# Kernel tuning notes

Hardware: AMD Instinct MI355X
Metric: run time of the kernel (lower is better)

## Reference

```python
import jax, jax.numpy as jnp
import numpy as np

N = 50000          # padded nodes
E_CFG = 800000     # padded cfg edges
E_GKT = 800000     # padded gkt edges
FN = 128           # node feature dim
FE = 128           # gkt edge feature dim
OUT = 128          # out_size (== hidden dim, required by shared Linears)
HEADS = 8
HEAD = OUT // HEADS
DIN = FN + OUT     # input dim to shared Linears


def _seg_softmax(logits, seg_ids, num_segments):
    mx = jax.ops.segment_max(logits, seg_ids, num_segments=num_segments)
    e = jnp.exp(logits - mx[seg_ids])
    s = jax.ops.segment_sum(e, seg_ids, num_segments=num_segments)
    return e / s[seg_ids]


def setup_inputs() -> dict:
    key = jax.random.key(0)
    ks = jax.random.split(key, 16)
    d = {
        'node_fts': jax.random.normal(ks[0], (N, FN), jnp.float32),
        'gkt_edge_fts': jax.random.normal(ks[1], (E_GKT, FE), jnp.float32),
        'hidden': jax.random.normal(ks[2], (N, OUT), jnp.float32),
        'cfg_indices_padded': jax.random.randint(ks[3], (E_CFG, 2), 0, N, jnp.int32),
        'gkt_indices_padded': jax.random.randint(ks[4], (E_GKT, 2), 0, N, jnp.int32),
    }
    sc = 1.0 / np.sqrt(DIN)
    d['W_m'] = jax.random.normal(ks[5], (DIN, OUT), jnp.float32) * sc
    d['b_m'] = jnp.zeros((OUT,), jnp.float32)
    d['W_skip'] = jax.random.normal(ks[6], (DIN, OUT), jnp.float32) * sc
    d['b_skip'] = jnp.zeros((OUT,), jnp.float32)
    d['W_a1'] = jax.random.normal(ks[7], (DIN, HEADS), jnp.float32) * sc
    d['b_a1'] = jnp.zeros((HEADS,), jnp.float32)
    d['W_a2'] = jax.random.normal(ks[8], (DIN, HEADS), jnp.float32) * sc
    d['b_a2'] = jnp.zeros((HEADS,), jnp.float32)
    d['W_ae'] = jax.random.normal(ks[9], (FE, HEADS), jnp.float32) * (1.0 / np.sqrt(FE))
    d['b_ae'] = jnp.zeros((HEADS,), jnp.float32)
    return d


def reference(node_fts, gkt_edge_fts, hidden, cfg_indices_padded, gkt_indices_padded,
              W_m, b_m, W_skip, b_skip, W_a1, b_a1, W_a2, b_a2, W_ae, b_ae):
    nb_nodes = node_fts.shape[0]
    nb_cfg = cfg_indices_padded.shape[0]
    nb_gkt = gkt_indices_padded.shape[0]
    cfg_row, cfg_col = cfg_indices_padded[:, 0], cfg_indices_padded[:, 1]
    gkt_row, gkt_col = gkt_indices_padded[:, 0], gkt_indices_padded[:, 1]

    # ---- cfg pass ----
    cfg_z = jnp.concatenate([node_fts, hidden], axis=-1)           # [N, DIN]
    cfg_att1 = cfg_z @ W_a1 + b_a1                                 # [N, H]
    cfg_att2 = cfg_z @ W_a2 + b_a2
    cfg_logits = cfg_att1[cfg_row] + cfg_att2[cfg_col]             # [E, H]
    cfg_coefs = _seg_softmax(jax.nn.leaky_relu(cfg_logits), cfg_row, nb_cfg)
    cfg_vals = (cfg_z @ W_m + b_m).reshape(nb_nodes, HEADS, HEAD)  # [N, H, hd]
    cfg_msg = cfg_coefs[:, :, None] * cfg_vals[cfg_col]            # [E, H, hd]
    cfg_hidden = jax.ops.segment_sum(cfg_msg, cfg_row, num_segments=nb_nodes)
    cfg_hidden = cfg_hidden.reshape(nb_nodes, OUT)
    cfg_hidden = cfg_hidden + (cfg_z @ W_skip + b_skip)            # residual
    cfg_hidden = jax.nn.relu(cfg_hidden)

    # ---- gkt pass ----
    gkt_z = jnp.concatenate([node_fts, cfg_hidden], axis=-1)       # [N, DIN]
    gkt_att1 = gkt_z @ W_a1 + b_a1
    gkt_att2 = gkt_z @ W_a2 + b_a2
    gkt_att_e = gkt_edge_fts @ W_ae + b_ae                         # [E, H]
    gkt_logits = gkt_att1[gkt_row] + gkt_att2[gkt_col] + gkt_att_e
    gkt_coefs = _seg_softmax(jax.nn.leaky_relu(gkt_logits), gkt_row, nb_gkt)
    gkt_vals = (gkt_z @ W_m + b_m).reshape(nb_nodes, HEADS, HEAD)
    msg = gkt_coefs[:, :, None] * gkt_vals[gkt_col]
    ret = jax.ops.segment_sum(msg, gkt_row, num_segments=nb_nodes)
    ret = ret.reshape(nb_nodes, OUT)
    ret = ret + (gkt_z @ W_skip + b_skip)
    ret = jax.nn.relu(ret)
    return ret
```

## Files before the change

kernel.cpp:

```cpp
#include <hip/hip_runtime.h>

using short8  = __attribute__((ext_vector_type(8))) short;
using floatx4 = __attribute__((ext_vector_type(4))) float;

#define CAP 64

__device__ __forceinline__ unsigned short f2bf(float f) {
    unsigned int u = __float_as_uint(f);
    u += 0x7fffu + ((u >> 16) & 1u);
    return (unsigned short)(u >> 16);
}
__device__ __forceinline__ float bf2f(unsigned short s) {
    return __uint_as_float(((unsigned int)s) << 16);
}

__global__ void k_prep(const float* __restrict__ Wm, const float* __restrict__ Wsk,
                       const float* __restrict__ Wa1, const float* __restrict__ Wa2,
                       unsigned short* __restrict__ Wpack, float* __restrict__ Wa,
                       const float* __restrict__ nf, const float* __restrict__ hid,
                       unsigned short* __restrict__ zbf,
                       int* __restrict__ cur0, int* __restrict__ cur1, int N) {
    int id = blockIdx.x * 256 + threadIdx.x;
    if (id < 65536) {
        int col = id >> 8;
        int k = id & 255;
        float v = (col < 128) ? Wm[k * 128 + col] : Wsk[k * 128 + (col - 128)];
        Wpack[col * 256 + k] = f2bf(v);
        if (id < 256 * 16) {
            int kk = id >> 4, j = id & 15;
            Wa[kk * 16 + j] = (j < 8) ? Wa1[kk * 8 + j] : Wa2[kk * 8 + (j - 8)];
        }
    }
    if (id < N) { cur0[id] = id * CAP; cur1[id] = id * CAP; }
    if (id >= N * 32) return;
    int row = id >> 5;
    int c4 = (id & 31) * 4;
    float4 av = *(const float4*)&nf[row * 128 + c4];
    float4 bv = *(const float4*)&hid[row * 128 + c4];
    ushort4 pa; pa.x = f2bf(av.x); pa.y = f2bf(av.y); pa.z = f2bf(av.z); pa.w = f2bf(av.w);
    ushort4 pb; pb.x = f2bf(bv.x); pb.y = f2bf(bv.y); pb.z = f2bf(bv.z); pb.w = f2bf(bv.w);
    *(ushort4*)&zbf[row * 256 + c4] = pa;
    *(ushort4*)&zbf[row * 256 + 128 + c4] = pb;
}

__global__ void k_fill_both(const int* __restrict__ cfg_idx, const int* __restrict__ gkt_idx,
                            int* __restrict__ cur0, int* __restrict__ cur1,
                            int* __restrict__ ccol, int2* __restrict__ ce, int Ec, int Eg) {
    int e = blockIdx.x * 256 + threadIdx.x;
    if (e < Ec) {
        int r = cfg_idx[2 * e], c = cfg_idx[2 * e + 1];
        int p = atomicAdd(&cur0[r], 1);
        if (p < r * CAP + CAP) ccol[p] = c;
    }
    if (e < Eg) {
        int r = gkt_idx[2 * e], c = gkt_idx[2 * e + 1];
        int p = atomicAdd(&cur1[r], 1);
        if (p < r * CAP + CAP) { int2 v; v.x = c; v.y = e; ce[p] = v; }
    }
}

__launch_bounds__(256)
__global__ void k_gemm(const unsigned short* __restrict__ zbf,
                       const unsigned short* __restrict__ Wpack,
                       const float* __restrict__ bm, const float* __restrict__ bsk,
                       unsigned short* __restrict__ vals, float* __restrict__ skip, int M) {
    const int colblk = blockIdx.x;
    const int rowBase = blockIdx.y * 128;
    __shared__ short As[128 * 40];
    __shared__ short Bs[128 * 40];
    const int t = threadIdx.x;
    const int wid = t >> 6, lane = t & 63;
    const int wm = wid >> 1, wn = wid & 1;

    floatx4 acc[4][4];
#pragma unroll
    for (int i = 0; i < 4; i++)
#pragma unroll
        for (int j = 0; j < 4; j++) acc[i][j] = (floatx4){0.f, 0.f, 0.f, 0.f};

    const unsigned short* Bbase = Wpack + colblk * 128 * 256;
    const int kq = (lane >> 4) * 8;
    const int rr = lane & 15;

    for (int kt = 0; kt < 256; kt += 32) {
#pragma unroll
        for (int s = 0; s < 2; s++) {
            int ch = t + s * 256;
            int r = ch >> 2, c = ch & 3;
            int gr = rowBase + r; if (gr >= M) gr = M - 1;
            *(int4*)&As[r * 40 + c * 8] = *(const int4*)&zbf[gr * 256 + kt + c * 8];
            *(int4*)&Bs[r * 40 + c * 8] = *(const int4*)&Bbase[r * 256 + kt + c * 8];
        }
        __syncthreads();
        short8 af[4], bfm[4];
#pragma unroll
        for (int i = 0; i < 4; i++) af[i] = *(short8*)&As[(wm * 64 + i * 16 + rr) * 40 + kq];
#pragma unroll
        for (int j = 0; j < 4; j++) bfm[j] = *(short8*)&Bs[(wn * 64 + j * 16 + rr) * 40 + kq];
#pragma unroll
        for (int i = 0; i < 4; i++)
#pragma unroll
            for (int j = 0; j < 4; j++)
                acc[i][j] = __builtin_amdgcn_mfma_f32_16x16x32_bf16(af[i], bfm[j], acc[i][j], 0, 0, 0);
        __syncthreads();
    }

    const int rquad = lane >> 4, cidx = lane & 15;
#pragma unroll
    for (int i = 0; i < 4; i++) {
#pragma unroll
        for (int j = 0; j < 4; j++) {
            int gc = wn * 64 + j * 16 + cidx;
#pragma unroll
            for (int r = 0; r < 4; r++) {
                int gr = rowBase + wm * 64 + i * 16 + rquad * 4 + r;
                if (gr < M) {
                    float v = acc[i][j][r];
                    if (colblk == 0) vals[gr * 128 + gc] = f2bf(v + bm[gc]);
                    else             skip[gr * 128 + gc] = v + bsk[gc];
                }
            }
        }
    }
}

__launch_bounds__(256)
__global__ void k_att(const float* __restrict__ zA, const float* __restrict__ zB,
                      const float* __restrict__ Wa, const float* __restrict__ ba1,
                      const float* __restrict__ ba2, float* __restrict__ att, int N) {
    __shared__ float Ws[4096];
    int t = threadIdx.x;
#pragma unroll
    for (int s = 0; s < 16; s++) Ws[s * 256 + t] = Wa[s * 256 + t];
    __syncthreads();
    int node = blockIdx.x * 256 + t;
    if (node >= N) return;
    float acc[16];
#pragma unroll
    for (int j = 0; j < 16; j++) acc[j] = (j < 8) ? ba1[j] : ba2[j - 8];
    const float* a = &zA[node * 128];
    const float* b = &zB[node * 128];
    for (int k0 = 0; k0 < 128; k0 += 4) {
        float4 v = *(const float4*)&a[k0];
        float vv[4] = {v.x, v.y, v.z, v.w};
#pragma unroll
        for (int r = 0; r < 4; r++) {
            const float* w = &Ws[(k0 + r) * 16];
#pragma unroll
            for (int j = 0; j < 16; j++) acc[j] += vv[r] * w[j];
        }
    }
    for (int k0 = 0; k0 < 128; k0 += 4) {
        float4 v = *(const float4*)&b[k0];
        float vv[4] = {v.x, v.y, v.z, v.w};
#pragma unroll
        for (int r = 0; r < 4; r++) {
            const float* w = &Ws[(128 + k0 + r) * 16];
#pragma unroll
            for (int j = 0; j < 16; j++) acc[j] += vv[r] * w[j];
        }
    }
#pragma unroll
    for (int j = 0; j < 16; j++) att[node * 16 + j] = acc[j];
}

__launch_bounds__(256)
__global__ void k_atte(const float* __restrict__ ef, const float* __restrict__ Wae,
                       const float* __restrict__ bae, float* __restrict__ atte, int E) {
    __shared__ float Ws[1024];
    int t = threadIdx.x;
    for (int s = t; s < 1024; s += 256) Ws[s] = Wae[s];
    __syncthreads();
    int e = blockIdx.x * 256 + t;
    if (e >= E) return;
    float acc[8];
#pragma unroll
    for (int h = 0; h < 8; h++) acc[h] = bae[h];
    const float* row = &ef[e * 128];
    for (int k0 = 0; k0 < 128; k0 += 4) {
        float4 v = *(const float4*)&row[k0];
        float vv[4] = {v.x, v.y, v.z, v.w};
#pragma unroll
        for (int r = 0; r < 4; r++) {
            const float* w = &Ws[(k0 + r) * 8];
#pragma unroll
            for (int h = 0; h < 8; h++) acc[h] += vv[r] * w[h];
        }
    }
    float4 o0 = {acc[0], acc[1], acc[2], acc[3]};
    float4 o1 = {acc[4], acc[5], acc[6], acc[7]};
    *(float4*)&atte[e * 8] = o0;
    *(float4*)&atte[e * 8 + 4] = o1;
}

template <int PHASE>
__launch_bounds__(256)
__global__ void k_agg(const int* __restrict__ cursor,
                      const int* __restrict__ ccol, const int2* __restrict__ ce,
                      const float* __restrict__ att, const unsigned short* __restrict__ vals,
                      const float* __restrict__ skip, const float* __restrict__ atte,
                      unsigned short* __restrict__ zbf, float* __restrict__ cfgh,
                      float* __restrict__ out, int N) {
    int node = (blockIdx.x * 256 + threadIdx.x) >> 6;
    int lane = threadIdx.x & 63;
    if (node >= N) return;
    int h = lane >> 3;
    int f0 = lane * 2;
    int base = node * CAP;
    int cnt = cursor[node] - base;
    if (cnt > CAP) cnt = CAP;
    if (cnt < 0) cnt = 0;

    int mycol = 0, myeid = 0;
    if (lane < cnt) {
        if (PHASE == 0) mycol = ccol[base + lane];
        else { int2 v = ce[base + lane]; mycol = v.x; myeid = v.y; }
    }
    float a1 = att[node * 16 + h];
    float acc0 = 0.f, acc1 = 0.f, dsum = 0.f;
#pragma unroll 4
    for (int s = 0; s < cnt; s++) {
        int col = __shfl(mycol, s);
        float logit = a1 + att[col * 16 + 8 + h];
        if (PHASE == 1) {
            int eid = __shfl(myeid, s);
            logit += atte[eid * 8 + h];
        }
        float l = (logit >= 0.f) ? logit : 0.01f * logit;
        float w = __expf(l);
        dsum += w;
        unsigned int pv = *(const unsigned int*)&vals[col * 128 + f0];
        acc0 += w * bf2f((unsigned short)(pv & 0xffffu));
        acc1 += w * bf2f((unsigned short)(pv >> 16));
    }
    if (cnt > 0) {
        float inv = 1.f / dsum;
        acc0 *= inv; acc1 *= inv;
    }
    float r0 = acc0 + skip[node * 128 + f0];
    float r1 = acc1 + skip[node * 128 + f0 + 1];
    r0 = r0 > 0.f ? r0 : 0.f;
    r1 = r1 > 0.f ? r1 : 0.f;
    if (PHASE == 0) {
        unsigned int packed = ((unsigned int)f2bf(r1) << 16) | (unsigned int)f2bf(r0);
        *(unsigned int*)&zbf[node * 256 + 128 + f0] = packed;
        float2 fo = {r0, r1};
        *(float2*)&cfgh[node * 128 + f0] = fo;
    } else {
        float2 fo = {r0, r1};
        *(float2*)&out[node * 128 + f0] = fo;
    }
}

extern "C" void kernel_launch(void* const* d_in, const int* in_sizes, int n_in,
                              void* d_out, int out_size, void* d_ws, size_t ws_size,
                              hipStream_t stream) {
    const float* node_fts = (const float*)d_in[0];
    const float* gkt_ef   = (const float*)d_in[1];
    const float* hidden   = (const float*)d_in[2];
    const int*   cfg_idx  = (const int*)d_in[3];
    const int*   gkt_idx  = (const int*)d_in[4];
    const float* W_m  = (const float*)d_in[5];
    const float* b_m  = (const float*)d_in[6];
    const float* W_sk = (const float*)d_in[7];
    const float* b_sk = (const float*)d_in[8];
    const float* W_a1 = (const float*)d_in[9];
    const float* b_a1 = (const float*)d_in[10];
    const float* W_a2 = (const float*)d_in[11];
    const float* b_a2 = (const float*)d_in[12];
    const float* W_ae = (const float*)d_in[13];
    const float* b_ae = (const float*)d_in[14];

    const int N  = in_sizes[0] / 128;
    const int Ec = in_sizes[3] / 2;
    const int Eg = in_sizes[4] / 2;
    const int Emax = (Ec > Eg) ? Ec : Eg;

    char* ws = (char*)d_ws;
    size_t off = 0;
    auto alloc = [&](size_t bytes) -> void* {
        off = (off + 255) & ~(size_t)255;
        void* p = ws + off;
        off += bytes;
        return p;
    };
    unsigned short* zbf   = (unsigned short*)alloc((size_t)N * 256 * 2);
    unsigned short* vals  = (unsigned short*)alloc((size_t)N * 128 * 2);
    float* skip   = (float*)alloc((size_t)N * 128 * 4);
    float* cfgh   = (float*)alloc((size_t)N * 128 * 4);
    float* att    = (float*)alloc((size_t)N * 16 * 4);
    float* atte   = (float*)alloc((size_t)Eg * 8 * 4);
    unsigned short* Wpack = (unsigned short*)alloc(256 * 256 * 2);
    float* Wa     = (float*)alloc(256 * 16 * 4);
    int* cur0     = (int*)alloc((size_t)N * 4);
    int* cur1     = (int*)alloc((size_t)N * 4);
    int* ccol     = (int*)alloc((size_t)N * CAP * 4);
    int2* ce      = (int2*)alloc((size_t)N * CAP * 8);

    dim3 ggrid(2, (N + 127) / 128);

    k_prep<<<(N * 32 + 255) / 256, 256, 0, stream>>>(W_m, W_sk, W_a1, W_a2, Wpack, Wa,
                                                     node_fts, hidden, zbf, cur0, cur1, N);
    k_fill_both<<<(Emax + 255) / 256, 256, 0, stream>>>(cfg_idx, gkt_idx, cur0, cur1,
                                                        ccol, ce, Ec, Eg);
    k_atte<<<(Eg + 255) / 256, 256, 0, stream>>>(gkt_ef, W_ae, b_ae, atte, Eg);

    k_gemm<<<ggrid, 256, 0, stream>>>(zbf, Wpack, b_m, b_sk, vals, skip, N);
    k_att<<<(N + 255) / 256, 256, 0, stream>>>(node_fts, hidden, Wa, b_a1, b_a2, att, N);
    k_agg<0><<<(N * 64 + 255) / 256, 256, 0, stream>>>(cur0, ccol, nullptr, att, vals,
                                                       skip, nullptr, zbf, cfgh, nullptr, N);

    k_gemm<<<ggrid, 256, 0, stream>>>(zbf, Wpack, b_m, b_sk, vals, skip, N);
    k_att<<<(N + 255) / 256, 256, 0, stream>>>(node_fts, cfgh, Wa, b_a1, b_a2, att, N);
    k_agg<1><<<(N * 64 + 255) / 256, 256, 0, stream>>>(cur1, nullptr, ce, att, vals,
                                                       skip, atte, nullptr, nullptr,
                                                       (float*)d_out, N);
}
```

Measured before the change: 1.023 ms.

## Precompute per-edge softmax weights in CSR slots before aggregation

Moves the attention-logit and exp computation out of the aggregation loop into per-edge kernels that write weights directly into the CSR slot layout. The cfg weights are computed during the fill (after computing att earlier), and the gkt edge-feature projection is fused with logit and exp into one kernel that also skips edges beyond capacity. Aggregation then streams contiguous weights instead of gathering att rows and edge logits. This adds two large weight buffers (N*CAP*8 floats each) and a pos1 array, which means extra memory traffic and footprint.

```diff
diff --git a/kernel.cpp b/kernel.cpp
--- a/kernel.cpp
+++ b/kernel.cpp
@@ -43,20 +43,89 @@
     *(ushort4*)&zbf[row * 256 + 128 + c4] = pb;
 }
 
-__global__ void k_fill_both(const int* __restrict__ cfg_idx, const int* __restrict__ gkt_idx,
-                            int* __restrict__ cur0, int* __restrict__ cur1,
-                            int* __restrict__ ccol, int2* __restrict__ ce, int Ec, int Eg) {
+__global__ void k_fillw(const int* __restrict__ cfg_idx, const int* __restrict__ gkt_idx,
+                        int* __restrict__ cur0, int* __restrict__ cur1,
+                        int* __restrict__ ccol0, int* __restrict__ ccol1,
+                        int* __restrict__ pos1, const float* __restrict__ att0,
+                        float* __restrict__ w0, int Ec, int Eg) {
     int e = blockIdx.x * 256 + threadIdx.x;
     if (e < Ec) {
         int r = cfg_idx[2 * e], c = cfg_idx[2 * e + 1];
         int p = atomicAdd(&cur0[r], 1);
-        if (p < r * CAP + CAP) ccol[p] = c;
+        if (p < r * CAP + CAP) {
+            ccol0[p] = c;
+            float4 x0 = *(const float4*)&att0[r * 16];
+            float4 x1 = *(const float4*)&att0[r * 16 + 4];
+            float4 y0 = *(const float4*)&att0[c * 16 + 8];
+            float4 y1 = *(const float4*)&att0[c * 16 + 12];
+            float l[8] = {x0.x + y0.x, x0.y + y0.y, x0.z + y0.z, x0.w + y0.w,
+                          x1.x + y1.x, x1.y + y1.y, x1.z + y1.z, x1.w + y1.w};
+            float w[8];
+#pragma unroll
+            for (int h = 0; h < 8; h++) {
+                float ll = (l[h] >= 0.f) ? l[h] : 0.01f * l[h];
+                w[h] = __expf(ll);
+            }
+            float4 wa = {w[0], w[1], w[2], w[3]};
+            float4 wb = {w[4], w[5], w[6], w[7]};
+            *(float4*)&w0[p * 8] = wa;
+            *(float4*)&w0[p * 8 + 4] = wb;
+        }
     }
     if (e < Eg) {
         int r = gkt_idx[2 * e], c = gkt_idx[2 * e + 1];
         int p = atomicAdd(&cur1[r], 1);
-        if (p < r * CAP + CAP) { int2 v; v.x = c; v.y = e; ce[p] = v; }
-    }
+        if (p < r * CAP + CAP) ccol1[p] = c;
+        pos1[e] = p;
+    }
+}
+
+__launch_bounds__(256)
+__global__ void k_wgkt(const float* __restrict__ ef, const float* __restrict__ Wae,
+                       const float* __restrict__ bae, const int* __restrict__ gkt_idx,
+                       const int* __restrict__ pos1, const float* __restrict__ att1,
+                       float* __restrict__ w1, int E) {
+    __shared__ float Ws[1024];
+    int t = threadIdx.x;
+    for (int s = t; s < 1024; s += 256) Ws[s] = Wae[s];
+    __syncthreads();
+    int e = blockIdx.x * 256 + t;
+    if (e >= E) return;
+    int p = pos1[e];
+    int r = gkt_idx[2 * e], c = gkt_idx[2 * e + 1];
+    if (p >= r * CAP + CAP) return;
+    float acc[8];
+#pragma unroll
+    for (int h = 0; h < 8; h++) acc[h] = bae[h];
+    const float* row = &ef[(size_t)e * 128];
+    for (int k0 = 0; k0 < 128; k0 += 4) {
+        float4 v = *(const float4*)&row[k0];
+        float vv[4] = {v.x, v.y, v.z, v.w};
+#pragma unroll
+        for (int rr = 0; rr < 4; rr++) {
+            const float* w = &Ws[(k0 + rr) * 8];
+#pragma unroll
+            for (int h = 0; h < 8; h++) acc[h] += vv[rr] * w[h];
+        }
+    }
+    float4 x0 = *(const float4*)&att1[r * 16];
+    float4 x1 = *(const float4*)&att1[r * 16 + 4];
+    float4 y0 = *(const float4*)&att1[c * 16 + 8];
+    float4 y1 = *(const float4*)&att1[c * 16 + 12];
+    float l[8] = {acc[0] + x0.x + y0.x, acc[1] + x0.y + y0.y,
+                  acc[2] + x0.z + y0.z, acc[3] + x0.w + y0.w,
+                  acc[4] + x1.x + y1.x, acc[5] + x1.y + y1.y,
+                  acc[6] + x1.z + y1.z, acc[7] + x1.w + y1.w};
+    float w[8];
+#pragma unroll
+    for (int h = 0; h < 8; h++) {
+        float ll = (l[h] >= 0.f) ? l[h] : 0.01f * l[h];
+        w[h] = __expf(ll);
+    }
+    float4 wa = {w[0], w[1], w[2], w[3]};
+    float4 wb = {w[4], w[5], w[6], w[7]};
+    *(float4*)&w1[p * 8] = wa;
+    *(float4*)&w1[p * 8 + 4] = wb;
 }
 
 __launch_bounds__(256)
@@ -164,41 +233,12 @@
     for (int j = 0; j < 16; j++) att[node * 16 + j] = acc[j];
 }
 
-__launch_bounds__(256)
-__global__ void k_atte(const float* __restrict__ ef, const float* __restrict__ Wae,
-                       const float* __restrict__ bae, float* __restrict__ atte, int E) {
-    __shared__ float Ws[1024];
-    int t = threadIdx.x;
-    for (int s = t; s < 1024; s += 256) Ws[s] = Wae[s];
-    __syncthreads();
-    int e = blockIdx.x * 256 + t;
-    if (e >= E) return;
-    float acc[8];
-#pragma unroll
-    for (int h = 0; h < 8; h++) acc[h] = bae[h];
-    const float* row = &ef[e * 128];
-    for (int k0 = 0; k0 < 128; k0 += 4) {
-        float4 v = *(const float4*)&row[k0];
-        float vv[4] = {v.x, v.y, v.z, v.w};
-#pragma unroll
-        for (int r = 0; r < 4; r++) {
-            const float* w = &Ws[(k0 + r) * 8];
-#pragma unroll
-            for (int h = 0; h < 8; h++) acc[h] += vv[r] * w[h];
-        }
-    }
-    float4 o0 = {acc[0], acc[1], acc[2], acc[3]};
-    float4 o1 = {acc[4], acc[5], acc[6], acc[7]};
-    *(float4*)&atte[e * 8] = o0;
-    *(float4*)&atte[e * 8 + 4] = o1;
-}
-
 template <int PHASE>
 __launch_bounds__(256)
-__global__ void k_agg(const int* __restrict__ cursor,
-                      const int* __restrict__ ccol, const int2* __restrict__ ce,
-                      const float* __restrict__ att, const unsigned short* __restrict__ vals,
-                      const float* __restrict__ skip, const float* __restrict__ atte,
+__global__ void k_agg(const int* __restrict__ cursor, const int* __restrict__ ccol,
+                      const float* __restrict__ wbuf,
+                      const unsigned short* __restrict__ vals,
+                      const float* __restrict__ skip,
                       unsigned short* __restrict__ zbf, float* __restrict__ cfgh,
                       float* __restrict__ out, int N) {
     int node = (blockIdx.x * 256 + threadIdx.x) >> 6;
@@ -211,27 +251,18 @@
     if (cnt > CAP) cnt = CAP;
     if (cnt < 0) cnt = 0;
 
-    int mycol = 0, myeid = 0;
-    if (lane < cnt) {
-        if (PHASE == 0) mycol = ccol[base + lane];
-        else { int2 v = ce[base + lane]; mycol = v.x; myeid = v.y; }
-    }
-    float a1 = att[node * 16 + h];
+    int mycol = 0;
+    if (lane < cnt) mycol = ccol[base + lane];
+    const float* wrow = &wbuf[base * 8 + h];
     float acc0 = 0.f, acc1 = 0.f, dsum = 0.f;
 #pragma unroll 4
     for (int s = 0; s < cnt; s++) {
         int col = __shfl(mycol, s);
-        float logit = a1 + att[col * 16 + 8 + h];
-        if (PHASE == 1) {
-            int eid = __shfl(myeid, s);
-            logit += atte[eid * 8 + h];
-        }
-        float l = (logit >= 0.f) ? logit : 0.01f * logit;
-        float w = __expf(l);
-        dsum += w;
+        float w = wrow[s * 8];
         unsigned int pv = *(const unsigned int*)&vals[col * 128 + f0];
         acc0 += w * bf2f((unsigned short)(pv & 0xffffu));
         acc1 += w * bf2f((unsigned short)(pv >> 16));
+        dsum += w;
     }
     if (cnt > 0) {
         float inv = 1.f / dsum;
@@ -289,30 +320,32 @@
     float* skip   = (float*)alloc((size_t)N * 128 * 4);
     float* cfgh   = (float*)alloc((size_t)N * 128 * 4);
     float* att    = (float*)alloc((size_t)N * 16 * 4);
-    float* atte   = (float*)alloc((size_t)Eg * 8 * 4);
     unsigned short* Wpack = (unsigned short*)alloc(256 * 256 * 2);
     float* Wa     = (float*)alloc(256 * 16 * 4);
     int* cur0     = (int*)alloc((size_t)N * 4);
     int* cur1     = (int*)alloc((size_t)N * 4);
-    int* ccol     = (int*)alloc((size_t)N * CAP * 4);
-    int2* ce      = (int2*)alloc((size_t)N * CAP * 8);
+    int* ccol0    = (int*)alloc((size_t)N * CAP * 4);
+    int* ccol1    = (int*)alloc((size_t)N * CAP * 4);
+    int* pos1     = (int*)alloc((size_t)Eg * 4);
+    float* w0     = (float*)alloc((size_t)N * CAP * 8 * 4);
+    float* w1     = (float*)alloc((size_t)N * CAP * 8 * 4);
 
     dim3 ggrid(2, (N + 127) / 128);
 
     k_prep<<<(N * 32 + 255) / 256, 256, 0, stream>>>(W_m, W_sk, W_a1, W_a2, Wpack, Wa,
                                                      node_fts, hidden, zbf, cur0, cur1, N);
-    k_fill_both<<<(Emax + 255) / 256, 256, 0, stream>>>(cfg_idx, gkt_idx, cur0, cur1,
-                                                        ccol, ce, Ec, Eg);
-    k_atte<<<(Eg + 255) / 256, 256, 0, stream>>>(gkt_ef, W_ae, b_ae, atte, Eg);
+    k_att<<<(N + 255) / 256, 256, 0, stream>>>(node_fts, hidden, Wa, b_a1, b_a2, att, N);
+    k_fillw<<<(Emax + 255) / 256, 256, 0, stream>>>(cfg_idx, gkt_idx, cur0, cur1,
+                                                    ccol0, ccol1, pos1, att, w0, Ec, Eg);
 
     k_gemm<<<ggrid, 256, 0, stream>>>(zbf, Wpack, b_m, b_sk, vals, skip, N);
-    k_att<<<(N + 255) / 256, 256, 0, stream>>>(node_fts, hidden, Wa, b_a1, b_a2, att, N);
-    k_agg<0><<<(N * 64 + 255) / 256, 256, 0, stream>>>(cur0, ccol, nullptr, att, vals,
-                                                       skip, nullptr, zbf, cfgh, nullptr, N);
-
+    k_agg<0><<<(N * 64 + 255) / 256, 256, 0, stream>>>(cur0, ccol0, w0, vals, skip,
+                                                       zbf, cfgh, nullptr, N);
+
+    k_att<<<(N + 255) / 256, 256, 0, stream>>>(node_fts, cfgh, Wa, b_a1, b_a2, att, N);
+    k_wgkt<<<(Eg + 255) / 256, 256, 0, stream>>>(gkt_ef, W_ae, b_ae, gkt_idx, pos1,
+                                                 att, w1, Eg);
     k_gemm<<<ggrid, 256, 0, stream>>>(zbf, Wpack, b_m, b_sk, vals, skip, N);
-    k_att<<<(N + 255) / 256, 256, 0, stream>>>(node_fts, cfgh, Wa, b_a1, b_a2, att, N);
-    k_agg<1><<<(N * 64 + 255) / 256, 256, 0, stream>>>(cur1, nullptr, ce, att, vals,
-                                                       skip, atte, nullptr, nullptr,
-                                                       (float*)d_out, N);
-}
+    k_agg<1><<<(N * 64 + 255) / 256, 256, 0, stream>>>(cur1, ccol1, w1, vals, skip,
+                                                       nullptr, nullptr, (float*)d_out, N);
+}
```

Result: no change. 1.009 ms (-1.3%).
